# Kernel optimization log

Hardware: AMD Instinct MI355X
Metric: run time of the kernel (lower is better)

The kernel has to match this reference:

```python
import jax, jax.numpy as jnp
import numpy as np

N_NODES = 100000
N_EDGES = 1600000
D_IN = 128
D_OUT = 128


def setup_inputs() -> dict:
    key = jax.random.key(0)
    k1, k2, k3 = jax.random.split(key, 3)
    x = jax.random.normal(k1, (N_NODES, D_IN), dtype=jnp.float32)
    edge_index = jax.random.randint(k2, (2, N_EDGES), 0, N_NODES, dtype=jnp.int64)
    # Xavier-uniform-like init for weight (matches nn.init.xavier_uniform_ scale)
    limit = float(np.sqrt(6.0 / (D_IN + D_OUT)))
    weight = jax.random.uniform(k3, (D_IN, D_OUT), dtype=jnp.float32,
                                minval=-limit, maxval=limit)
    bias = jnp.zeros((D_OUT,), dtype=jnp.float32)
    return {"x": x, "edge_index": edge_index, "weight": weight, "bias": bias}


def reference(x, edge_index, weight, bias):
    num_nodes = x.shape[0]
    src = edge_index[0]  # edge_index_i: gather side
    dst = edge_index[1]  # edge_index_j: scatter side

    # Degree of each node counted over src endpoints.
    deg = jax.ops.segment_sum(jnp.ones_like(src, dtype=x.dtype), src,
                              num_segments=num_nodes)
    # deg^{-1/2} with inf -> 0 for isolated nodes.
    deg_safe = jnp.where(deg > 0, deg, jnp.ones_like(deg))
    deg_inv_sqrt = jnp.where(deg > 0, jax.lax.rsqrt(deg_safe), jnp.zeros_like(deg))

    norm = deg_inv_sqrt[src] * deg_inv_sqrt[dst]  # [E]

    h = x @ weight  # [N, D_OUT]
    # Edge-parallel gather, scale, scatter-add.
    msgs = norm[:, None] * h[src]  # [E, D_OUT]
    out = jax.ops.segment_sum(msgs, dst, num_segments=num_nodes)  # [N, D_OUT]
    return out + bias
```

## Files before the change

kernel.cpp:

```cpp
#include <hip/hip_runtime.h>

#define D 128
#define CAP 64
#define NCHUNK 128
#define MAXW 25088
#define CURW 12544
#define LDW 136
#define LDO 132

typedef __attribute__((ext_vector_type(8))) short bf16x8;
typedef __attribute__((ext_vector_type(4))) float f32x4;

__device__ __forceinline__ unsigned f2bf(float f) {
    unsigned u = __float_as_uint(f);
    return (u + 0x7fffu + ((u >> 16) & 1u)) >> 16;
}

__device__ __forceinline__ int chunk_size(int n_edges) {
    return (((n_edges + NCHUNK - 1) / NCHUNK) + 3) & ~3;
}

__global__ __launch_bounds__(1024) void k_hist(const int* __restrict__ src,
                                               const int* __restrict__ dst,
                                               unsigned* __restrict__ pb_s,
                                               unsigned* __restrict__ pb_d,
                                               int n_edges, int wtot) {
    __shared__ unsigned h[MAXW];
    int chunk = blockIdx.x & (NCHUNK - 1);
    int role  = blockIdx.x >> 7;
    const int* ids = role ? src : dst;
    unsigned* pb   = role ? pb_s : pb_d;
    int tid = threadIdx.x;
    for (int i = tid; i < wtot; i += 1024) h[i] = 0;
    __syncthreads();

    int csz = chunk_size(n_edges);
    int beg = chunk * csz;
    int end = min(beg + csz, n_edges);
    if (beg < end) {
        int aend = beg + ((end - beg) & ~3);
        for (int i = beg + tid * 4; i + 3 < aend; i += 4096) {
            int4 v = *(const int4*)(ids + i);
            unsigned b;
            b = (unsigned)v.x; atomicAdd(&h[b >> 2], 1u << ((b & 3) * 8));
            b = (unsigned)v.y; atomicAdd(&h[b >> 2], 1u << ((b & 3) * 8));
            b = (unsigned)v.z; atomicAdd(&h[b >> 2], 1u << ((b & 3) * 8));
            b = (unsigned)v.w; atomicAdd(&h[b >> 2], 1u << ((b & 3) * 8));
        }
        for (int e = aend + tid; e < end; e += 1024) {
            unsigned b = (unsigned)ids[e];
            atomicAdd(&h[b >> 2], 1u << ((b & 3) * 8));
        }
    }
    __syncthreads();
    unsigned* p = pb + (size_t)chunk * wtot;
    for (int i = tid; i < wtot; i += 1024) p[i] = h[i];
}

__global__ __launch_bounds__(1024) void k_scan(unsigned* __restrict__ pb_d,
                                               const unsigned* __restrict__ pb_s,
                                               int* __restrict__ deg_dst,
                                               float* __restrict__ dis,
                                               int n, int wtot) {
    int lane = threadIdx.x & 63;
    int gw = blockIdx.x * 16 + (threadIdx.x >> 6);
    if (gw < wtot) {
        int w = gw;
        unsigned v0 = pb_d[(size_t)(2 * lane) * wtot + w];
        unsigned v1 = pb_d[(size_t)(2 * lane + 1) * wtot + w];
        unsigned s = v0 + v1;
        unsigned inc = s;
        #pragma unroll
        for (int off = 1; off < 64; off <<= 1) {
            unsigned t = __shfl_up(inc, off, 64);
            if (lane >= off) inc += t;
        }
        unsigned excl = inc - s;
        pb_d[(size_t)(2 * lane) * wtot + w] = excl;
        pb_d[(size_t)(2 * lane + 1) * wtot + w] = excl + v0;
        unsigned tot = __shfl(inc, 63, 64);
        if (lane == 0) {
            int g0 = w * 4;
            int d0 = tot & 0xffu, d1 = (tot >> 8) & 0xffu,
                d2 = (tot >> 16) & 0xffu, d3 = (tot >> 24) & 0xffu;
            if (g0 + 3 < n) {
                *(int4*)(deg_dst + g0) = make_int4(d0, d1, d2, d3);
            } else {
                int dd[4] = {d0, d1, d2, d3};
                #pragma unroll
                for (int j = 0; j < 4; ++j)
                    if (g0 + j < n) deg_dst[g0 + j] = dd[j];
            }
        }
    } else if (gw < 2 * wtot) {
        int w = gw - wtot;
        unsigned s = pb_s[(size_t)(2 * lane) * wtot + w] +
                     pb_s[(size_t)(2 * lane + 1) * wtot + w];
        #pragma unroll
        for (int off = 1; off < 64; off <<= 1) s += __shfl_xor(s, off, 64);
        if (lane == 0) {
            int g0 = w * 4;
            unsigned s0 = s & 0xffu, s1 = (s >> 8) & 0xffu,
                     s2 = (s >> 16) & 0xffu, s3 = (s >> 24) & 0xffu;
            if (g0 + 3 < n) {
                *(float4*)(dis + g0) = make_float4(
                    s0 ? rsqrtf((float)s0) : 0.0f, s1 ? rsqrtf((float)s1) : 0.0f,
                    s2 ? rsqrtf((float)s2) : 0.0f, s3 ? rsqrtf((float)s3) : 0.0f);
            } else {
                unsigned ssx[4] = {s0, s1, s2, s3};
                #pragma unroll
                for (int j = 0; j < 4; ++j)
                    if (g0 + j < n) dis[g0 + j] = ssx[j] ? rsqrtf((float)ssx[j]) : 0.0f;
            }
        }
    }
}

__global__ __launch_bounds__(1024) void k_place(const int* __restrict__ src,
                                                const int* __restrict__ dst,
                                                const unsigned* __restrict__ pb_d,
                                                int* __restrict__ epad,
                                                int n_edges, int wtot) {
    __shared__ unsigned cur[CURW];
    int half  = blockIdx.x >> 7;
    int chunk = blockIdx.x & (NCHUNK - 1);
    int tid = threadIdx.x;
    int wtot2 = (wtot + 1) >> 1;
    int wb = half * wtot2;
    int wcnt = min(wtot2, wtot - wb);
    const unsigned* cb = pb_d + (size_t)chunk * wtot + wb;
    for (int i = tid; i < wcnt; i += 1024) cur[i] = cb[i];
    __syncthreads();

    int csz = chunk_size(n_edges);
    int beg = chunk * csz;
    int end = min(beg + csz, n_edges);
    if (beg < end) {
        int aend = beg + ((end - beg) & ~3);
        for (int i = beg + tid * 4; i + 3 < aend; i += 4096) {
            int4 s = *(const int4*)(src + i);
            int4 d = *(const int4*)(dst + i);
            unsigned b, wrel, o, r;
            b = (unsigned)d.x; wrel = (b >> 2) - wb;
            if (wrel < (unsigned)wcnt) {
                o = atomicAdd(&cur[wrel], 1u << ((b & 3) * 8));
                r = (o >> ((b & 3) * 8)) & 0xffu;
                if (r < CAP) epad[((size_t)b << 6) + r] = s.x;
            }
            b = (unsigned)d.y; wrel = (b >> 2) - wb;
            if (wrel < (unsigned)wcnt) {
                o = atomicAdd(&cur[wrel], 1u << ((b & 3) * 8));
                r = (o >> ((b & 3) * 8)) & 0xffu;
                if (r < CAP) epad[((size_t)b << 6) + r] = s.y;
            }
            b = (unsigned)d.z; wrel = (b >> 2) - wb;
            if (wrel < (unsigned)wcnt) {
                o = atomicAdd(&cur[wrel], 1u << ((b & 3) * 8));
                r = (o >> ((b & 3) * 8)) & 0xffu;
                if (r < CAP) epad[((size_t)b << 6) + r] = s.z;
            }
            b = (unsigned)d.w; wrel = (b >> 2) - wb;
            if (wrel < (unsigned)wcnt) {
                o = atomicAdd(&cur[wrel], 1u << ((b & 3) * 8));
                r = (o >> ((b & 3) * 8)) & 0xffu;
                if (r < CAP) epad[((size_t)b << 6) + r] = s.w;
            }
        }
        for (int e = aend + tid; e < end; e += 1024) {
            unsigned b = (unsigned)dst[e];
            unsigned wrel = (b >> 2) - wb;
            if (wrel < (unsigned)wcnt) {
                unsigned o = atomicAdd(&cur[wrel], 1u << ((b & 3) * 8));
                unsigned r = (o >> ((b & 3) * 8)) & 0xffu;
                if (r < CAP) epad[((size_t)b << 6) + r] = src[e];
            }
        }
    }
}

__global__ __launch_bounds__(256) void k_gemm(const float* __restrict__ x,
                                              const float* __restrict__ w,
                                              const float* __restrict__ dis,
                                              unsigned* __restrict__ hb, int nrows) {
    __shared__ __align__(16) unsigned short wt[128][LDW];
    __shared__ __align__(16) float sOut[4][16][LDO];
    int tid = threadIdx.x;

    {
        const float4* w4 = (const float4*)w;
        #pragma unroll
        for (int it = 0; it < 16; ++it) {
            int i = tid + it * 256;
            int k = i >> 5, n0 = (i & 31) * 4;
            float4 v = w4[i];
            wt[n0 + 0][k] = (unsigned short)f2bf(v.x);
            wt[n0 + 1][k] = (unsigned short)f2bf(v.y);
            wt[n0 + 2][k] = (unsigned short)f2bf(v.z);
            wt[n0 + 3][k] = (unsigned short)f2bf(v.w);
        }
    }
    __syncthreads();

    int lane = tid & 63, wv = tid >> 6;
    int m = lane & 15, quad = lane >> 4;
    int rbase = blockIdx.x * 128 + wv * 32;

    int r0 = rbase + m, r1 = rbase + 16 + m;
    const float* pa0 = x + (size_t)(r0 < nrows ? r0 : 0) * D;
    const float* pa1 = x + (size_t)(r1 < nrows ? r1 : 0) * D;

    f32x4 acc[2][8] = {};
    #pragma unroll
    for (int kt = 0; kt < 4; ++kt) {
        int k0 = kt * 32 + quad * 8;
        float4 a0l = *(const float4*)(pa0 + k0);
        float4 a0h = *(const float4*)(pa0 + k0 + 4);
        float4 a1l = *(const float4*)(pa1 + k0);
        float4 a1h = *(const float4*)(pa1 + k0 + 4);
        bf16x8 a0, a1;
        a0[0] = (short)f2bf(a0l.x); a0[1] = (short)f2bf(a0l.y);
        a0[2] = (short)f2bf(a0l.z); a0[3] = (short)f2bf(a0l.w);
        a0[4] = (short)f2bf(a0h.x); a0[5] = (short)f2bf(a0h.y);
        a0[6] = (short)f2bf(a0h.z); a0[7] = (short)f2bf(a0h.w);
        a1[0] = (short)f2bf(a1l.x); a1[1] = (short)f2bf(a1l.y);
        a1[2] = (short)f2bf(a1l.z); a1[3] = (short)f2bf(a1l.w);
        a1[4] = (short)f2bf(a1h.x); a1[5] = (short)f2bf(a1h.y);
        a1[6] = (short)f2bf(a1h.z); a1[7] = (short)f2bf(a1h.w);
        bf16x8 b[8];
        #pragma unroll
        for (int ct = 0; ct < 8; ++ct)
            b[ct] = *(const bf16x8*)&wt[ct * 16 + m][k0];
        #pragma unroll
        for (int ct = 0; ct < 8; ++ct) {
            acc[0][ct] = __builtin_amdgcn_mfma_f32_16x16x32_bf16(a0, b[ct], acc[0][ct], 0, 0, 0);
            acc[1][ct] = __builtin_amdgcn_mfma_f32_16x16x32_bf16(a1, b[ct], acc[1][ct], 0, 0, 0);
        }
    }

    float* so = &sOut[wv][0][0];
    int ri = lane >> 2, qc = lane & 3;
    #pragma unroll
    for (int rt = 0; rt < 2; ++rt) {
        #pragma unroll
        for (int ct = 0; ct < 8; ++ct)
            #pragma unroll
            for (int reg = 0; reg < 4; ++reg)
                so[(quad * 4 + reg) * LDO + ct * 16 + m] = acc[rt][ct][reg];
        int row = rbase + rt * 16 + ri;
        if (row < nrows) {
            float dn = dis[row];
            const float* sr = so + ri * LDO + qc * 32;
            unsigned* hrow = hb + (size_t)row * 64 + qc * 16;
            #pragma unroll
            for (int j = 0; j < 4; ++j) {
                float2 p0 = *(const float2*)(sr + j * 8 + 0);
                float2 p1 = *(const float2*)(sr + j * 8 + 2);
                float2 p2 = *(const float2*)(sr + j * 8 + 4);
                float2 p3 = *(const float2*)(sr + j * 8 + 6);
                uint4 o;
                o.x = f2bf(dn * p0.x) | (f2bf(dn * p0.y) << 16);
                o.y = f2bf(dn * p1.x) | (f2bf(dn * p1.y) << 16);
                o.z = f2bf(dn * p2.x) | (f2bf(dn * p2.y) << 16);
                o.w = f2bf(dn * p3.x) | (f2bf(dn * p3.y) << 16);
                *(uint4*)(hrow + j * 4) = o;
            }
        }
        __builtin_amdgcn_s_waitcnt(0);
    }
}

#define ACC8(u) do { \
    ax[0] += __uint_as_float((u).x << 16); ax[1] += __uint_as_float((u).x & 0xffff0000u); \
    ax[2] += __uint_as_float((u).y << 16); ax[3] += __uint_as_float((u).y & 0xffff0000u); \
    ax[4] += __uint_as_float((u).z << 16); ax[5] += __uint_as_float((u).z & 0xffff0000u); \
    ax[6] += __uint_as_float((u).w << 16); ax[7] += __uint_as_float((u).w & 0xffff0000u); } while (0)

__global__ __launch_bounds__(256) void k_accum(const int* __restrict__ epad,
                                               const int* __restrict__ degd,
                                               const uint4* __restrict__ hb4,
                                               const float* __restrict__ dis,
                                               const float* __restrict__ bias,
                                               float* __restrict__ out, int n) {
    int wid = threadIdx.x >> 6, lane = threadIdx.x & 63;
    int node = blockIdx.x * 4 + wid;
    if (node >= n) return;
    int deg = min(degd[node], CAP);
    int g = lane >> 4, c = lane & 15;
    const int* ep = epad + (size_t)node * CAP;

    float ax[8] = {0.f, 0.f, 0.f, 0.f, 0.f, 0.f, 0.f, 0.f};
    int e = g;
    for (; e + 12 < deg; e += 16) {
        int s0 = ep[e];
        int s1 = ep[e + 4];
        int s2 = ep[e + 8];
        int s3 = ep[e + 12];
        uint4 u0 = hb4[(size_t)s0 * 16 + c];
        uint4 u1 = hb4[(size_t)s1 * 16 + c];
        uint4 u2 = hb4[(size_t)s2 * 16 + c];
        uint4 u3 = hb4[(size_t)s3 * 16 + c];
        ACC8(u0); ACC8(u1); ACC8(u2); ACC8(u3);
    }
    for (; e < deg; e += 4) {
        int s0 = ep[e];
        uint4 u0 = hb4[(size_t)s0 * 16 + c];
        ACC8(u0);
    }

    #pragma unroll
    for (int k = 0; k < 8; ++k) {
        ax[k] += __shfl_xor(ax[k], 16, 64);
        ax[k] += __shfl_xor(ax[k], 32, 64);
    }

    if (g == 0) {
        float dn = dis[node];
        float4 b0 = ((const float4*)bias)[c * 2];
        float4 b1 = ((const float4*)bias)[c * 2 + 1];
        float4 o0 = make_float4(fmaf(dn, ax[0], b0.x), fmaf(dn, ax[1], b0.y),
                                fmaf(dn, ax[2], b0.z), fmaf(dn, ax[3], b0.w));
        float4 o1 = make_float4(fmaf(dn, ax[4], b1.x), fmaf(dn, ax[5], b1.y),
                                fmaf(dn, ax[6], b1.z), fmaf(dn, ax[7], b1.w));
        float4* op = (float4*)(out + (size_t)node * D) + c * 2;
        op[0] = o0;
        op[1] = o1;
    }
}

extern "C" void kernel_launch(void* const* d_in, const int* in_sizes, int n_in,
                              void* d_out, int out_size, void* d_ws, size_t ws_size,
                              hipStream_t stream) {
    const float* x    = (const float*)d_in[0];
    const int*   ei   = (const int*)d_in[1];
    const float* w    = (const float*)d_in[2];
    const float* bias = (const float*)d_in[3];
    float* out = (float*)d_out;

    int n_edges = in_sizes[1] / 2;
    int n_nodes = in_sizes[0] / D;
    const int* src = ei;
    const int* dst = ei + n_edges;

    int wtot = (n_nodes + 3) / 4;

    char* ws = (char*)d_ws;
    unsigned* hb = (unsigned*)ws;      ws += (size_t)n_nodes * 64 * sizeof(unsigned);
    int* epad    = (int*)ws;           ws += (size_t)n_nodes * CAP * sizeof(int);
    int* deg_dst = (int*)ws;           ws += (size_t)n_nodes * sizeof(int);
    float* dis   = (float*)ws;         ws += (size_t)n_nodes * sizeof(float);
    unsigned* pb_s = (unsigned*)ws;    ws += (size_t)NCHUNK * wtot * sizeof(unsigned);
    unsigned* pb_d = (unsigned*)ws;

    k_hist<<<2 * NCHUNK, 1024, 0, stream>>>(src, dst, pb_s, pb_d, n_edges, wtot);
    k_scan<<<(2 * wtot + 15) / 16, 1024, 0, stream>>>(pb_d, pb_s, deg_dst, dis,
                                                      n_nodes, wtot);
    k_gemm<<<(n_nodes + 127) / 128, 256, 0, stream>>>(x, w, dis, hb, n_nodes);
    k_place<<<2 * NCHUNK, 1024, 0, stream>>>(src, dst, pb_d, epad, n_edges, wtot);
    k_accum<<<(n_nodes + 3) / 4, 256, 0, stream>>>(epad, deg_dst, (const uint4*)hb,
                                                   dis, bias, out, n_nodes);
}
```

Measured before the change: 250.3 us.

## Use single-pass full-range placement and 512-thread hist/place blocks; vectorize weight transpose

The placement kernel stops splitting each edge chunk into two node-range halves. Each of 128 blocks now loads the full per-chunk cursor table into LDS and places every edge once, which removes the duplicated reads of src/dst and the range checks. The histogram and placement kernels drop from 1024 to 512 threads per block. The GEMM weight staging now writes packed bf16 pairs with 8-byte LDS stores instead of scalar transposed stores, but its global reads become strided. The trade-off is half as many placement blocks, each using about 100KB of LDS, so fewer threads are in flight for the atomic scatter.

```diff
diff --git a/kernel.cpp b/kernel.cpp
--- a/kernel.cpp
+++ b/kernel.cpp
@@ -4,7 +4,6 @@
 #define CAP 64
 #define NCHUNK 128
 #define MAXW 25088
-#define CURW 12544
 #define LDW 136
 #define LDO 132
 
@@ -20,18 +19,18 @@
     return (((n_edges + NCHUNK - 1) / NCHUNK) + 3) & ~3;
 }
 
-__global__ __launch_bounds__(1024) void k_hist(const int* __restrict__ src,
-                                               const int* __restrict__ dst,
-                                               unsigned* __restrict__ pb_s,
-                                               unsigned* __restrict__ pb_d,
-                                               int n_edges, int wtot) {
+__global__ __launch_bounds__(512) void k_hist(const int* __restrict__ src,
+                                              const int* __restrict__ dst,
+                                              unsigned* __restrict__ pb_s,
+                                              unsigned* __restrict__ pb_d,
+                                              int n_edges, int wtot) {
     __shared__ unsigned h[MAXW];
-    int chunk = blockIdx.x & (NCHUNK - 1);
-    int role  = blockIdx.x >> 7;
+    int chunk = blockIdx.x % NCHUNK;
+    int role  = blockIdx.x / NCHUNK;
     const int* ids = role ? src : dst;
     unsigned* pb   = role ? pb_s : pb_d;
     int tid = threadIdx.x;
-    for (int i = tid; i < wtot; i += 1024) h[i] = 0;
+    for (int i = tid; i < wtot; i += 512) h[i] = 0;
     __syncthreads();
 
     int csz = chunk_size(n_edges);
@@ -39,7 +38,7 @@
     int end = min(beg + csz, n_edges);
     if (beg < end) {
         int aend = beg + ((end - beg) & ~3);
-        for (int i = beg + tid * 4; i + 3 < aend; i += 4096) {
+        for (int i = beg + tid * 4; i + 3 < aend; i += 2048) {
             int4 v = *(const int4*)(ids + i);
             unsigned b;
             b = (unsigned)v.x; atomicAdd(&h[b >> 2], 1u << ((b & 3) * 8));
@@ -47,14 +46,14 @@
             b = (unsigned)v.z; atomicAdd(&h[b >> 2], 1u << ((b & 3) * 8));
             b = (unsigned)v.w; atomicAdd(&h[b >> 2], 1u << ((b & 3) * 8));
         }
-        for (int e = aend + tid; e < end; e += 1024) {
+        for (int e = aend + tid; e < end; e += 512) {
             unsigned b = (unsigned)ids[e];
             atomicAdd(&h[b >> 2], 1u << ((b & 3) * 8));
         }
     }
     __syncthreads();
     unsigned* p = pb + (size_t)chunk * wtot;
-    for (int i = tid; i < wtot; i += 1024) p[i] = h[i];
+    for (int i = tid; i < wtot; i += 512) p[i] = h[i];
 }
 
 __global__ __launch_bounds__(1024) void k_scan(unsigned* __restrict__ pb_d,
@@ -116,20 +115,16 @@
     }
 }
 
-__global__ __launch_bounds__(1024) void k_place(const int* __restrict__ src,
-                                                const int* __restrict__ dst,
-                                                const unsigned* __restrict__ pb_d,
-                                                int* __restrict__ epad,
-                                                int n_edges, int wtot) {
-    __shared__ unsigned cur[CURW];
-    int half  = blockIdx.x >> 7;
-    int chunk = blockIdx.x & (NCHUNK - 1);
+__global__ __launch_bounds__(512) void k_place(const int* __restrict__ src,
+                                               const int* __restrict__ dst,
+                                               const unsigned* __restrict__ pb_d,
+                                               int* __restrict__ epad,
+                                               int n_edges, int wtot) {
+    __shared__ unsigned cur[MAXW];
+    int chunk = blockIdx.x;
     int tid = threadIdx.x;
-    int wtot2 = (wtot + 1) >> 1;
-    int wb = half * wtot2;
-    int wcnt = min(wtot2, wtot - wb);
-    const unsigned* cb = pb_d + (size_t)chunk * wtot + wb;
-    for (int i = tid; i < wcnt; i += 1024) cur[i] = cb[i];
+    const unsigned* cb = pb_d + (size_t)chunk * wtot;
+    for (int i = tid; i < wtot; i += 512) cur[i] = cb[i];
     __syncthreads();
 
     int csz = chunk_size(n_edges);
@@ -137,43 +132,32 @@
     int end = min(beg + csz, n_edges);
     if (beg < end) {
         int aend = beg + ((end - beg) & ~3);
-        for (int i = beg + tid * 4; i + 3 < aend; i += 4096) {
+        for (int i = beg + tid * 4; i + 3 < aend; i += 2048) {
             int4 s = *(const int4*)(src + i);
             int4 d = *(const int4*)(dst + i);
-            unsigned b, wrel, o, r;
-            b = (unsigned)d.x; wrel = (b >> 2) - wb;
-            if (wrel < (unsigned)wcnt) {
-                o = atomicAdd(&cur[wrel], 1u << ((b & 3) * 8));
-                r = (o >> ((b & 3) * 8)) & 0xffu;
-                if (r < CAP) epad[((size_t)b << 6) + r] = s.x;
-            }
-            b = (unsigned)d.y; wrel = (b >> 2) - wb;
-            if (wrel < (unsigned)wcnt) {
-                o = atomicAdd(&cur[wrel], 1u << ((b & 3) * 8));
-                r = (o >> ((b & 3) * 8)) & 0xffu;
-                if (r < CAP) epad[((size_t)b << 6) + r] = s.y;
-            }
-            b = (unsigned)d.z; wrel = (b >> 2) - wb;
-            if (wrel < (unsigned)wcnt) {
-                o = atomicAdd(&cur[wrel], 1u << ((b & 3) * 8));
-                r = (o >> ((b & 3) * 8)) & 0xffu;
-                if (r < CAP) epad[((size_t)b << 6) + r] = s.z;
-            }
-            b = (unsigned)d.w; wrel = (b >> 2) - wb;
-            if (wrel < (unsigned)wcnt) {
-                o = atomicAdd(&cur[wrel], 1u << ((b & 3) * 8));
-                r = (o >> ((b & 3) * 8)) & 0xffu;
-                if (r < CAP) epad[((size_t)b << 6) + r] = s.w;
-            }
-        }
-        for (int e = aend + tid; e < end; e += 1024) {
+            unsigned b, o, r;
+            b = (unsigned)d.x;
+            o = atomicAdd(&cur[b >> 2], 1u << ((b & 3) * 8));
+            r = (o >> ((b & 3) * 8)) & 0xffu;
+            if (r < CAP) epad[((size_t)b << 6) + r] = s.x;
+            b = (unsigned)d.y;
+            o = atomicAdd(&cur[b >> 2], 1u << ((b & 3) * 8));
+            r = (o >> ((b & 3) * 8)) & 0xffu;
+            if (r < CAP) epad[((size_t)b << 6) + r] = s.y;
+            b = (unsigned)d.z;
+            o = atomicAdd(&cur[b >> 2], 1u << ((b & 3) * 8));
+            r = (o >> ((b & 3) * 8)) & 0xffu;
+            if (r < CAP) epad[((size_t)b << 6) + r] = s.z;
+            b = (unsigned)d.w;
+            o = atomicAdd(&cur[b >> 2], 1u << ((b & 3) * 8));
+            r = (o >> ((b & 3) * 8)) & 0xffu;
+            if (r < CAP) epad[((size_t)b << 6) + r] = s.w;
+        }
+        for (int e = aend + tid; e < end; e += 512) {
             unsigned b = (unsigned)dst[e];
-            unsigned wrel = (b >> 2) - wb;
-            if (wrel < (unsigned)wcnt) {
-                unsigned o = atomicAdd(&cur[wrel], 1u << ((b & 3) * 8));
-                unsigned r = (o >> ((b & 3) * 8)) & 0xffu;
-                if (r < CAP) epad[((size_t)b << 6) + r] = src[e];
-            }
+            unsigned o = atomicAdd(&cur[b >> 2], 1u << ((b & 3) * 8));
+            unsigned r = (o >> ((b & 3) * 8)) & 0xffu;
+            if (r < CAP) epad[((size_t)b << 6) + r] = src[e];
         }
     }
 }
@@ -187,16 +171,18 @@
     int tid = threadIdx.x;
 
     {
-        const float4* w4 = (const float4*)w;
+        int k0 = (tid & 31) * 4;
+        int nb = tid >> 5;
         #pragma unroll
         for (int it = 0; it < 16; ++it) {
-            int i = tid + it * 256;
-            int k = i >> 5, n0 = (i & 31) * 4;
-            float4 v = w4[i];
-            wt[n0 + 0][k] = (unsigned short)f2bf(v.x);
-            wt[n0 + 1][k] = (unsigned short)f2bf(v.y);
-            wt[n0 + 2][k] = (unsigned short)f2bf(v.z);
-            wt[n0 + 3][k] = (unsigned short)f2bf(v.w);
+            int n = nb + it * 8;
+            float va = w[(k0 + 0) * D + n];
+            float vb = w[(k0 + 1) * D + n];
+            float vc = w[(k0 + 2) * D + n];
+            float vd = w[(k0 + 3) * D + n];
+            unsigned lo = f2bf(va) | (f2bf(vb) << 16);
+            unsigned hi = f2bf(vc) | (f2bf(vd) << 16);
+            *(uint2*)&wt[n][k0] = make_uint2(lo, hi);
         }
     }
     __syncthreads();
@@ -351,11 +337,11 @@
     unsigned* pb_s = (unsigned*)ws;    ws += (size_t)NCHUNK * wtot * sizeof(unsigned);
     unsigned* pb_d = (unsigned*)ws;
 
-    k_hist<<<2 * NCHUNK, 1024, 0, stream>>>(src, dst, pb_s, pb_d, n_edges, wtot);
+    k_hist<<<2 * NCHUNK, 512, 0, stream>>>(src, dst, pb_s, pb_d, n_edges, wtot);
     k_scan<<<(2 * wtot + 15) / 16, 1024, 0, stream>>>(pb_d, pb_s, deg_dst, dis,
                                                       n_nodes, wtot);
     k_gemm<<<(n_nodes + 127) / 128, 256, 0, stream>>>(x, w, dis, hb, n_nodes);
-    k_place<<<2 * NCHUNK, 1024, 0, stream>>>(src, dst, pb_d, epad, n_edges, wtot);
+    k_place<<<NCHUNK, 512, 0, stream>>>(src, dst, pb_d, epad, n_edges, wtot);
     k_accum<<<(n_nodes + 3) / 4, 256, 0, stream>>>(epad, deg_dst, (const uint4*)hb,
                                                    dis, bias, out, n_nodes);
 }
```

Result: slower. 269.0 us (+7.5%).
